# Kernel optimization log

Measured on AMD Instinct MI355X. Metric: run time of the kernel, lower is better.

The kernel has to match this reference:

```python
import jax, jax.numpy as jnp
import numpy as np

B, C, H, WID = 32, 64, 128, 128
K = 5            # co-occurrence bins (co_shape)
WH = 3           # spatial filter height/width (w_shape = (1,3,3), depth 1)
ACT_LO, ACT_HI = 0.0, 1.0  # actBounds


def setup_inputs() -> dict:
    key = jax.random.key(0)
    k1, k2, k3 = jax.random.split(key, 3)
    input_tensor = jax.random.uniform(k1, (B, C, H, WID), dtype=jnp.float32)
    # learned params: L ~ N(0, 0.1) of shape (k,k); W ~ N(0,0.1) of shape (d,h,w)
    L = 0.1 * jax.random.normal(k2, (K, K), dtype=jnp.float32)
    W = 0.1 * jax.random.normal(k3, (1, WH, WH), dtype=jnp.float32)
    return {"input_tensor": input_tensor, "W": W, "L": L}


def _quantize(x, k):
    # map activation in [ACT_LO, ACT_HI] to bin index in [0, k-1]
    b = jnp.floor((x - ACT_LO) / (ACT_HI - ACT_LO) * k)
    return jnp.clip(b, 0, k - 1).astype(jnp.int32)


def reference(input_tensor, W, L):
    """Co-occurrence layer:
    out[p] = sum_{q in 3x3 nbhd(p)} W[q-p] * L[bin(x[q]), bin(x[p])] * x[q]
    Out-of-bounds neighbors contribute 0 (zero pad => x[q]=0 kills the term),
    matching the precomputed neighbor_lookup_table boundary handling.
    """
    k = L.shape[0]
    pad = WH // 2
    bins = _quantize(input_tensor, k)                      # (B,C,H,W) int32
    xp = jnp.pad(input_tensor, ((0, 0), (0, 0), (pad, pad), (pad, pad)))
    bp = jnp.pad(bins, ((0, 0), (0, 0), (pad, pad), (pad, pad)))
    h, w = input_tensor.shape[2], input_tensor.shape[3]
    out = jnp.zeros_like(input_tensor)
    for dh in range(WH):                                   # tiny fixed 3x3 loop
        for dw in range(WH):
            xn = xp[:, :, dh:dh + h, dw:dw + w]            # shifted neighbor values
            bn = bp[:, :, dh:dh + h, dw:dw + w]            # shifted neighbor bins
            out = out + W[0, dh, dw] * L[bn, bins] * xn    # gather L + weighted acc
    return out
```

## Files before the change

kernel.cpp:

```cpp
#include <hip/hip_runtime.h>


namespace {
constexpr int H  = 128;
constexpr int WD = 128;
constexpr int PLANES = 32 * 64;
constexpr int PX = 8;
constexpr int THREADS = 256;
}

__global__ __launch_bounds__(THREADS, 5) void col_kernel(
    const float* __restrict__ x, const float* __restrict__ Wf,
    const float* __restrict__ Lf, float* __restrict__ out)
{
    __shared__ float WL[9 * 25];
    const int t = threadIdx.x;
    if (t < 225) WL[t] = Wf[t / 25] * Lf[t % 25];
    __syncthreads();

    const int col0 = (t & 15) * PX;
    const int r0   = (t >> 4) * 8;

    const float* xp = x + (size_t)blockIdx.x * (H * WD);
    float* opb      = out + (size_t)blockIdx.x * (H * WD);
    const char* wlb = (const char*)WL;

    float win[3][PX + 2];
    int   pk[3][3];

#define LOAD_ROW(S, RR) {                                                 \
    const int _rr = (RR);                                                 \
    if (_rr >= 0 && _rr < H) {                                            \
        const float* _rp = xp + _rr * WD + col0;                          \
        const float4 _c0 = *(const float4*)_rp;          \
        const float4 _c1 = *(const float4*)(_rp + 4);                     \
        win[S][0] = (col0 > 0) ? _rp[-1] : 0.f;                           \
        win[S][1] = _c0.x; win[S][2] = _c0.y;                             \
        win[S][3] = _c0.z; win[S][4] = _c0.w;                             \
        win[S][5] = _c1.x; win[S][6] = _c1.y;                             \
        win[S][7] = _c1.z; win[S][8] = _c1.w;                             \
        win[S][9] = (col0 < WD - PX) ? _rp[PX] : 0.f;                     \
    } else {                                                              \
        _Pragma("unroll")                                                 \
        for (int _j = 0; _j < PX + 2; ++_j) win[S][_j] = 0.f;             \
    } }

#define QPACK(S) {                                                        \
    int _b[PX + 2];                                                       \
    _Pragma("unroll")                                                     \
    for (int _j = 0; _j < PX + 2; ++_j) {                                 \
        int _v = (int)(win[S][_j] * 5.0f);        \
        _v = (_v > 4) ? 4 : _v;                                           \
        _b[_j] = _v * 20;                                                 \
    }                                                                     \
    pk[S][0] = _b[0] | (_b[1] << 8) | (_b[2] << 16) | (_b[3] << 24);      \
    pk[S][1] = _b[4] | (_b[5] << 8) | (_b[6] << 16) | (_b[7] << 24);      \
    pk[S][2] = _b[8] | (_b[9] << 8); }

#define BF(S, J) ((pk[S][(J) >> 2] >> (8 * ((J) & 3))) & 0xff)

#define TERMS(QS, DR) {                                                   \
    _Pragma("unroll")                                                     \
    for (int _dw = 0; _dw < 3; ++_dw) {                                   \
        float _lw[PX];                                                    \
        _Pragma("unroll")                                                 \
        for (int _i = 0; _i < PX; ++_i)                                   \
            _lw[_i] = *(const float*)(wlb +                               \
                (BF(QS, _i + _dw) + bp4[_i] + ((DR) * 3 + _dw) * 100));   \
        _Pragma("unroll")                                                 \
        for (int _i = 0; _i < PX; ++_i)                                   \
            acc[_i] = fmaf(_lw[_i], win[QS][_i + _dw], acc[_i]);          \
    } }

#define COMPUTE(A, B, C, R) {                                             \
    int bp4[PX];                                                          \
    _Pragma("unroll")                                                     \
    for (int _i = 0; _i < PX; ++_i)                                       \
        bp4[_i] = (BF(B, _i + 1) * 52429) >> 18;         \
    float acc[PX];                                                        \
    _Pragma("unroll")                                                     \
    for (int _i = 0; _i < PX; ++_i) acc[_i] = 0.f;                        \
    TERMS(A, 0)                                                           \
    TERMS(B, 1)                                                           \
    TERMS(C, 2)                                                           \
    float* _op = opb + (R) * WD + col0;                                   \
    *(float4*)_op       = make_float4(acc[0], acc[1], acc[2], acc[3]);    \
    *(float4*)(_op + 4) = make_float4(acc[4], acc[5], acc[6], acc[7]);    \
    }

    LOAD_ROW(0, r0 - 1) QPACK(0)
    LOAD_ROW(1, r0 + 0) QPACK(1)
    LOAD_ROW(2, r0 + 1) QPACK(2)

    COMPUTE(0, 1, 2, r0 + 0)  LOAD_ROW(0, r0 + 2) QPACK(0)
    COMPUTE(1, 2, 0, r0 + 1)  LOAD_ROW(1, r0 + 3) QPACK(1)
    COMPUTE(2, 0, 1, r0 + 2)  LOAD_ROW(2, r0 + 4) QPACK(2)
    COMPUTE(0, 1, 2, r0 + 3)  LOAD_ROW(0, r0 + 5) QPACK(0)
    COMPUTE(1, 2, 0, r0 + 4)  LOAD_ROW(1, r0 + 6) QPACK(1)
    COMPUTE(2, 0, 1, r0 + 5)  LOAD_ROW(2, r0 + 7) QPACK(2)
    COMPUTE(0, 1, 2, r0 + 6)  LOAD_ROW(0, r0 + 8) QPACK(0)
    COMPUTE(1, 2, 0, r0 + 7)

#undef LOAD_ROW
#undef QPACK
#undef BF
#undef TERMS
#undef COMPUTE
}

extern "C" void kernel_launch(void* const* d_in, const int* in_sizes, int n_in,
                              void* d_out, int out_size, void* d_ws, size_t ws_size,
                              hipStream_t stream) {
    const float* x  = (const float*)d_in[0];
    const float* Wf = (const float*)d_in[1];
    const float* Lf = (const float*)d_in[2];
    float* out = (float*)d_out;

    col_kernel<<<dim3(PLANES), dim3(THREADS), 0, stream>>>(x, Wf, Lf, out);
}
```

Before: 253.7 us.

## Software-pipeline LDS table gathers against FMAs with double-buffered registers

Restructures the per-row compute into a software pipeline. The LDS gathers of the W*L products for the next tap row go into one register buffer while FMAs consume the other, and sched_barrier calls pin this interleaving. The next row's global load and quantisation are placed inside this schedule, and the first gather group is hoisted before the loop. Occupancy hint is lowered from 5 to 4 waves to make room for the extra registers, at the cost of less latency hiding across waves.

```diff
diff --git a/kernel.cpp b/kernel.cpp
--- a/kernel.cpp
+++ b/kernel.cpp
@@ -9,7 +9,7 @@
 constexpr int THREADS = 256;
 }
 
-__global__ __launch_bounds__(THREADS, 5) void col_kernel(
+__global__ __launch_bounds__(THREADS, 4) void col_kernel(
     const float* __restrict__ x, const float* __restrict__ Wf,
     const float* __restrict__ Lf, float* __restrict__ out)
 {
@@ -27,6 +27,11 @@
 
     float win[3][PX + 2];
     int   pk[3][3];
+    float lw0[24], lw1[24];
+    float acc[PX];
+    int   bp4[PX];
+
+#define SB __builtin_amdgcn_sched_barrier(0);
 
 #define LOAD_ROW(S, RR) {                                                 \
     const int _rr = (RR);                                                 \
@@ -59,53 +64,79 @@
 
 #define BF(S, J) ((pk[S][(J) >> 2] >> (8 * ((J) & 3))) & 0xff)
 
-#define TERMS(QS, DR) {                                                   \
+#define BP4(B) {                                                          \
+    _Pragma("unroll")                                                     \
+    for (int _i = 0; _i < PX; ++_i)                                       \
+        bp4[_i] = (BF(B, _i + 1) * 52429) >> 18; }
+
+#define GS(LW, QS, DR) {                                                  \
     _Pragma("unroll")                                                     \
     for (int _dw = 0; _dw < 3; ++_dw) {                                   \
-        float _lw[PX];                                                    \
         _Pragma("unroll")                                                 \
         for (int _i = 0; _i < PX; ++_i)                                   \
-            _lw[_i] = *(const float*)(wlb +                               \
+            LW[_dw * 8 + _i] = *(const float*)(wlb +                      \
                 (BF(QS, _i + _dw) + bp4[_i] + ((DR) * 3 + _dw) * 100));   \
+    } }
+
+#define FS(LW, QS) {                                                      \
+    _Pragma("unroll")                                                     \
+    for (int _dw = 0; _dw < 3; ++_dw) {                                   \
         _Pragma("unroll")                                                 \
         for (int _i = 0; _i < PX; ++_i)                                   \
-            acc[_i] = fmaf(_lw[_i], win[QS][_i + _dw], acc[_i]);          \
+            acc[_i] = fmaf(LW[_dw * 8 + _i], win[QS][_i + _dw], acc[_i]); \
     } }
 
-#define COMPUTE(A, B, C, R) {                                             \
-    int bp4[PX];                                                          \
+#define ZACC {                                                            \
     _Pragma("unroll")                                                     \
-    for (int _i = 0; _i < PX; ++_i)                                       \
-        bp4[_i] = (BF(B, _i + 1) * 52429) >> 18;         \
-    float acc[PX];                                                        \
-    _Pragma("unroll")                                                     \
-    for (int _i = 0; _i < PX; ++_i) acc[_i] = 0.f;                        \
-    TERMS(A, 0)                                                           \
-    TERMS(B, 1)                                                           \
-    TERMS(C, 2)                                                           \
+    for (int _i = 0; _i < PX; ++_i) acc[_i] = 0.f; }
+
+#define STORE(R) {                                                        \
     float* _op = opb + (R) * WD + col0;                                   \
     *(float4*)_op       = make_float4(acc[0], acc[1], acc[2], acc[3]);    \
     *(float4*)(_op + 4) = make_float4(acc[4], acc[5], acc[6], acc[7]);    \
     }
 
+#define STEP(PA, PB, PC, R, X, Y)                                         \
+    GS(Y, PB, 1) SB                                                       \
+    ZACC FS(X, PA) LOAD_ROW(PA, (R) + 2) SB                               \
+    GS(X, PC, 2) SB                                                       \
+    FS(Y, PB) QPACK(PA) BP4(PC) SB                                        \
+    GS(Y, PB, 0) SB                                                       \
+    FS(X, PC) STORE(R)
+
+#define STEPLAST(PA, PB, PC, R, X, Y)                                     \
+    GS(Y, PB, 1) SB                                                       \
+    ZACC FS(X, PA) SB                                                     \
+    GS(X, PC, 2) SB                                                       \
+    FS(Y, PB) SB                                                          \
+    FS(X, PC) STORE(R)
+
     LOAD_ROW(0, r0 - 1) QPACK(0)
     LOAD_ROW(1, r0 + 0) QPACK(1)
     LOAD_ROW(2, r0 + 1) QPACK(2)
+    BP4(1)
+    GS(lw0, 0, 0) SB
 
-    COMPUTE(0, 1, 2, r0 + 0)  LOAD_ROW(0, r0 + 2) QPACK(0)
-    COMPUTE(1, 2, 0, r0 + 1)  LOAD_ROW(1, r0 + 3) QPACK(1)
-    COMPUTE(2, 0, 1, r0 + 2)  LOAD_ROW(2, r0 + 4) QPACK(2)
-    COMPUTE(0, 1, 2, r0 + 3)  LOAD_ROW(0, r0 + 5) QPACK(0)
-    COMPUTE(1, 2, 0, r0 + 4)  LOAD_ROW(1, r0 + 6) QPACK(1)
-    COMPUTE(2, 0, 1, r0 + 5)  LOAD_ROW(2, r0 + 7) QPACK(2)
-    COMPUTE(0, 1, 2, r0 + 6)  LOAD_ROW(0, r0 + 8) QPACK(0)
-    COMPUTE(1, 2, 0, r0 + 7)
+    STEP(0, 1, 2, r0 + 0, lw0, lw1)
+    STEP(1, 2, 0, r0 + 1, lw1, lw0)
+    STEP(2, 0, 1, r0 + 2, lw0, lw1)
+    STEP(0, 1, 2, r0 + 3, lw1, lw0)
+    STEP(1, 2, 0, r0 + 4, lw0, lw1)
+    STEP(2, 0, 1, r0 + 5, lw1, lw0)
+    STEP(0, 1, 2, r0 + 6, lw0, lw1)
+    STEPLAST(1, 2, 0, r0 + 7, lw1, lw0)
 
+#undef SB
 #undef LOAD_ROW
 #undef QPACK
 #undef BF
-#undef TERMS
-#undef COMPUTE
+#undef BP4
+#undef GS
+#undef FS
+#undef ZACC
+#undef STORE
+#undef STEP
+#undef STEPLAST
 }
 
 extern "C" void kernel_launch(void* const* d_in, const int* in_sizes, int n_in,
```

Measured after the change: 411.9 us. 62.4% more time.

## Compute one output row per thread across two planes with interleaved gathers

Applied to the files above, without the earlier changes.

Replaces the per-plane block with row-sliding-window reuse by blocks covering 8-row tiles. Each thread computes 4 pixels of a single row for two planes, interleaving shared-memory gathers of one plane with FMAs of the other to hide LDS latency. This exposes more blocks and independent work but drops the vertical window reuse, so every output row reloads its three input rows (about 3x global/L2 read traffic) and the grid grows to 16384 blocks.

```diff
diff --git a/kernel.cpp b/kernel.cpp
--- a/kernel.cpp
+++ b/kernel.cpp
@@ -4,12 +4,14 @@
 namespace {
 constexpr int H  = 128;
 constexpr int WD = 128;
-constexpr int PLANES = 32 * 64;
-constexpr int PX = 8;
+constexpr int PPT = 4;
 constexpr int THREADS = 256;
+constexpr int ROWS_PB = 8;
+constexpr int TILES = H / ROWS_PB;
+constexpr int PAIRS = 1024;
 }
 
-__global__ __launch_bounds__(THREADS, 5) void col_kernel(
+__global__ __launch_bounds__(THREADS, 4) void col_kernel(
     const float* __restrict__ x, const float* __restrict__ Wf,
     const float* __restrict__ Lf, float* __restrict__ out)
 {
@@ -18,94 +20,108 @@
     if (t < 225) WL[t] = Wf[t / 25] * Lf[t % 25];
     __syncthreads();
 
-    const int col0 = (t & 15) * PX;
-    const int r0   = (t >> 4) * 8;
+    const int cs  = (t & 31) * PPT;
+    const int row = (blockIdx.x & 15) * ROWS_PB + (t >> 5);
+    const int pA  = blockIdx.x >> 4;
 
-    const float* xp = x + (size_t)blockIdx.x * (H * WD);
-    float* opb      = out + (size_t)blockIdx.x * (H * WD);
+    const float* xa = x + (size_t)pA * (H * WD);
+    const float* xb = x + (size_t)(pA + PAIRS) * (H * WD);
+    float* oa = out + (size_t)pA * (H * WD) + row * WD + cs;
+    float* ob = out + (size_t)(pA + PAIRS) * (H * WD) + row * WD + cs;
     const char* wlb = (const char*)WL;
 
-    float win[3][PX + 2];
-    int   pk[3][3];
+    float winA[3][PPT + 2], winB[3][PPT + 2];
+    int   pkA[3][2],        pkB[3][2];
+    int   bp4A[PPT],        bp4B[PPT];
+    float lwA[12],          lwB[12];
+    float accA[PPT],        accB[PPT];
 
-#define LOAD_ROW(S, RR) {                                                 \
+#define LOAD_ROW(WR, XP, RR) {                                            \
     const int _rr = (RR);                                                 \
     if (_rr >= 0 && _rr < H) {                                            \
-        const float* _rp = xp + _rr * WD + col0;                          \
-        const float4 _c0 = *(const float4*)_rp;          \
-        const float4 _c1 = *(const float4*)(_rp + 4);                     \
-        win[S][0] = (col0 > 0) ? _rp[-1] : 0.f;                           \
-        win[S][1] = _c0.x; win[S][2] = _c0.y;                             \
-        win[S][3] = _c0.z; win[S][4] = _c0.w;                             \
-        win[S][5] = _c1.x; win[S][6] = _c1.y;                             \
-        win[S][7] = _c1.z; win[S][8] = _c1.w;                             \
-        win[S][9] = (col0 < WD - PX) ? _rp[PX] : 0.f;                     \
+        const float* _rp = (XP) + _rr * WD + cs;                          \
+        const float4 _c = *(const float4*)_rp;           \
+        WR[0] = (cs > 0) ? _rp[-1] : 0.f;                                 \
+        WR[1] = _c.x; WR[2] = _c.y; WR[3] = _c.z; WR[4] = _c.w;           \
+        WR[5] = (cs < WD - PPT) ? _rp[PPT] : 0.f;                         \
     } else {                                                              \
         _Pragma("unroll")                                                 \
-        for (int _j = 0; _j < PX + 2; ++_j) win[S][_j] = 0.f;             \
+        for (int _j = 0; _j < PPT + 2; ++_j) WR[_j] = 0.f;                \
     } }
 
-#define QPACK(S) {                                                        \
-    int _b[PX + 2];                                                       \
+#define QPACK(WR, PK) {                                                   \
+    int _b[PPT + 2];                                                      \
     _Pragma("unroll")                                                     \
-    for (int _j = 0; _j < PX + 2; ++_j) {                                 \
-        int _v = (int)(win[S][_j] * 5.0f);        \
+    for (int _j = 0; _j < PPT + 2; ++_j) {                                \
+        int _v = (int)(WR[_j] * 5.0f);            \
         _v = (_v > 4) ? 4 : _v;                                           \
         _b[_j] = _v * 20;                                                 \
     }                                                                     \
-    pk[S][0] = _b[0] | (_b[1] << 8) | (_b[2] << 16) | (_b[3] << 24);      \
-    pk[S][1] = _b[4] | (_b[5] << 8) | (_b[6] << 16) | (_b[7] << 24);      \
-    pk[S][2] = _b[8] | (_b[9] << 8); }
+    PK[0] = _b[0] | (_b[1] << 8) | (_b[2] << 16) | (_b[3] << 24);         \
+    PK[1] = _b[4] | (_b[5] << 8); }
 
-#define BF(S, J) ((pk[S][(J) >> 2] >> (8 * ((J) & 3))) & 0xff)
+#define BF(PK, J) ((PK[(J) >> 2] >> (8 * ((J) & 3))) & 0xff)
 
-#define TERMS(QS, DR) {                                                   \
+#define BP4(PK1, BP) {                                                    \
+    _Pragma("unroll")                                                     \
+    for (int _i = 0; _i < PPT; ++_i)                                      \
+        BP[_i] = (BF(PK1, _i + 1) * 52429) >> 18;     }
+
+#define GS(LW, PK, BP, DR) {                                              \
     _Pragma("unroll")                                                     \
     for (int _dw = 0; _dw < 3; ++_dw) {                                   \
-        float _lw[PX];                                                    \
         _Pragma("unroll")                                                 \
-        for (int _i = 0; _i < PX; ++_i)                                   \
-            _lw[_i] = *(const float*)(wlb +                               \
-                (BF(QS, _i + _dw) + bp4[_i] + ((DR) * 3 + _dw) * 100));   \
-        _Pragma("unroll")                                                 \
-        for (int _i = 0; _i < PX; ++_i)                                   \
-            acc[_i] = fmaf(_lw[_i], win[QS][_i + _dw], acc[_i]);          \
+        for (int _i = 0; _i < PPT; ++_i)                                  \
+            LW[_dw * PPT + _i] = *(const float*)(wlb +                    \
+                (BF(PK[DR], _i + _dw) + BP[_i] + ((DR) * 3 + _dw) * 100));\
     } }
 
-#define COMPUTE(A, B, C, R) {                                             \
-    int bp4[PX];                                                          \
+#define FS(LW, WIN, ACC, DR) {                                            \
     _Pragma("unroll")                                                     \
-    for (int _i = 0; _i < PX; ++_i)                                       \
-        bp4[_i] = (BF(B, _i + 1) * 52429) >> 18;         \
-    float acc[PX];                                                        \
-    _Pragma("unroll")                                                     \
-    for (int _i = 0; _i < PX; ++_i) acc[_i] = 0.f;                        \
-    TERMS(A, 0)                                                           \
-    TERMS(B, 1)                                                           \
-    TERMS(C, 2)                                                           \
-    float* _op = opb + (R) * WD + col0;                                   \
-    *(float4*)_op       = make_float4(acc[0], acc[1], acc[2], acc[3]);    \
-    *(float4*)(_op + 4) = make_float4(acc[4], acc[5], acc[6], acc[7]);    \
-    }
+    for (int _dw = 0; _dw < 3; ++_dw) {                                   \
+        _Pragma("unroll")                                                 \
+        for (int _i = 0; _i < PPT; ++_i)                                  \
+            ACC[_i] = fmaf(LW[_dw * PPT + _i], WIN[DR][_i + _dw],         \
+                           ACC[_i]);                                      \
+    } }
 
-    LOAD_ROW(0, r0 - 1) QPACK(0)
-    LOAD_ROW(1, r0 + 0) QPACK(1)
-    LOAD_ROW(2, r0 + 1) QPACK(2)
+    LOAD_ROW(winA[0], xa, row - 1)
+    LOAD_ROW(winA[1], xa, row + 0)
+    LOAD_ROW(winA[2], xa, row + 1)
+    LOAD_ROW(winB[0], xb, row - 1)
+    LOAD_ROW(winB[1], xb, row + 0)
+    LOAD_ROW(winB[2], xb, row + 1)
 
-    COMPUTE(0, 1, 2, r0 + 0)  LOAD_ROW(0, r0 + 2) QPACK(0)
-    COMPUTE(1, 2, 0, r0 + 1)  LOAD_ROW(1, r0 + 3) QPACK(1)
-    COMPUTE(2, 0, 1, r0 + 2)  LOAD_ROW(2, r0 + 4) QPACK(2)
-    COMPUTE(0, 1, 2, r0 + 3)  LOAD_ROW(0, r0 + 5) QPACK(0)
-    COMPUTE(1, 2, 0, r0 + 4)  LOAD_ROW(1, r0 + 6) QPACK(1)
-    COMPUTE(2, 0, 1, r0 + 5)  LOAD_ROW(2, r0 + 7) QPACK(2)
-    COMPUTE(0, 1, 2, r0 + 6)  LOAD_ROW(0, r0 + 8) QPACK(0)
-    COMPUTE(1, 2, 0, r0 + 7)
+    QPACK(winA[0], pkA[0]) QPACK(winA[1], pkA[1]) QPACK(winA[2], pkA[2])
+    QPACK(winB[0], pkB[0]) QPACK(winB[1], pkB[1]) QPACK(winB[2], pkB[2])
+    BP4(pkA[1], bp4A)
+    BP4(pkB[1], bp4B)
+
+    #pragma unroll
+    for (int i = 0; i < PPT; ++i) { accA[i] = 0.f; accB[i] = 0.f; }
+
+    GS(lwA, pkA, bp4A, 0)
+    GS(lwB, pkB, bp4B, 0)
+    FS(lwA, winA, accA, 0)
+    GS(lwA, pkA, bp4A, 1)
+    FS(lwB, winB, accB, 0)
+    GS(lwB, pkB, bp4B, 1)
+    FS(lwA, winA, accA, 1)
+    GS(lwA, pkA, bp4A, 2)
+    FS(lwB, winB, accB, 1)
+    GS(lwB, pkB, bp4B, 2)
+    FS(lwA, winA, accA, 2)
+    FS(lwB, winB, accB, 2)
+
+    *(float4*)oa = make_float4(accA[0], accA[1], accA[2], accA[3]);
+    *(float4*)ob = make_float4(accB[0], accB[1], accB[2], accB[3]);
 
 #undef LOAD_ROW
 #undef QPACK
 #undef BF
-#undef TERMS
-#undef COMPUTE
+#undef BP4
+#undef GS
+#undef FS
 }
 
 extern "C" void kernel_launch(void* const* d_in, const int* in_sizes, int n_in,
@@ -116,5 +132,5 @@
     const float* Lf = (const float*)d_in[2];
     float* out = (float*)d_out;
 
-    col_kernel<<<dim3(PLANES), dim3(THREADS), 0, stream>>>(x, Wf, Lf, out);
+    col_kernel<<<dim3(PAIRS * TILES), dim3(THREADS), 0, stream>>>(x, Wf, Lf, out);
 }
```

Result: slower. 278.1 us (+9.6%).
